# Kernel optimization log

Hardware: AMD Instinct MI355X
Metric: run time of the kernel (lower is better)

## Reference

```python
import jax, jax.numpy as jnp
import numpy as np

N = 16384   # nodes
E = 262144  # edges (avg degree 16)
H = 256     # hidden_dim
R = 32      # num_radial


def _lin(k, fi, fo):
    return jax.random.normal(k, (fi, fo), jnp.float32) / np.float32(np.sqrt(fi))


def setup_inputs() -> dict:
    key = jax.random.key(0)
    ks = jax.random.split(key, 16)
    h = jax.random.normal(ks[0], (N, H), jnp.float32)
    pos = jax.random.normal(ks[1], (N, 3), jnp.float32)
    edge_index = jax.random.randint(ks[2], (2, E), 0, N, dtype=jnp.int32)
    return {
        'h': h, 'pos': pos,
        # radial_basis: Linear(1,R), SiLU, Linear(R,R)
        'rb_w1': _lin(ks[3], 1, R), 'rb_b1': jnp.zeros((R,), jnp.float32),
        'rb_w2': _lin(ks[4], R, R), 'rb_b2': jnp.zeros((R,), jnp.float32),
        # edge_network: Linear(2H+R,H), SiLU, Linear(H,H), LayerNorm(H)
        'en_w1': _lin(ks[5], 2 * H + R, H), 'en_b1': jnp.zeros((H,), jnp.float32),
        'en_w2': _lin(ks[6], H, H), 'en_b2': jnp.zeros((H,), jnp.float32),
        'en_g': jnp.ones((H,), jnp.float32), 'en_bt': jnp.zeros((H,), jnp.float32),
        # node_network: Linear(2H,H), SiLU, Linear(H,H), LayerNorm(H)
        'nn_w1': _lin(ks[7], 2 * H, H), 'nn_b1': jnp.zeros((H,), jnp.float32),
        'nn_w2': _lin(ks[8], H, H), 'nn_b2': jnp.zeros((H,), jnp.float32),
        'nn_g': jnp.ones((H,), jnp.float32), 'nn_bt': jnp.zeros((H,), jnp.float32),
        # coord_network: Linear(H,H//2), SiLU, Linear(H//2,1), Tanh
        'cn_w1': _lin(ks[9], H, H // 2), 'cn_b1': jnp.zeros((H // 2,), jnp.float32),
        'cn_w2': _lin(ks[10], H // 2, 1), 'cn_b2': jnp.zeros((1,), jnp.float32),
        'edge_index': edge_index,
    }


def _ln(x, g, b, eps=1e-5):
    mu = jnp.mean(x, axis=-1, keepdims=True)
    var = jnp.var(x, axis=-1, keepdims=True)
    return (x - mu) / jnp.sqrt(var + eps) * g + b


def reference(h, pos, rb_w1, rb_b1, rb_w2, rb_b2,
              en_w1, en_b1, en_w2, en_b2, en_g, en_bt,
              nn_w1, nn_b1, nn_w2, nn_b2, nn_g, nn_bt,
              cn_w1, cn_b1, cn_w2, cn_b2, edge_index):
    row, col = edge_index[0], edge_index[1]
    rel_pos = pos[col] - pos[row]                                   # [E,3]
    # torch: norm(rel_pos + 1e-8) -> scalar eps added to the vector first
    dist = jnp.linalg.norm(rel_pos + 1e-8, axis=-1, keepdims=True)  # [E,1]
    radial = jax.nn.silu(dist @ rb_w1 + rb_b1) @ rb_w2 + rb_b2      # [E,R]
    edge_feat = jnp.concatenate([h[row], h[col], radial], axis=-1)  # [E,2H+R]
    edge_msg = _ln(jax.nn.silu(edge_feat @ en_w1 + en_b1) @ en_w2 + en_b2,
                   en_g, en_bt)                                     # [E,H]
    # PyG propagate with aggr='add': sum messages at target nodes (col)
    node_msg = jax.ops.segment_sum(edge_msg, col, num_segments=h.shape[0])
    hn_in = jnp.concatenate([h, node_msg], axis=-1)                 # [N,2H]
    h_updated = _ln(jax.nn.silu(hn_in @ nn_w1 + nn_b1) @ nn_w2 + nn_b2,
                    nn_g, nn_bt)                                    # [N,H]
    coord_w = jnp.tanh(jax.nn.silu(edge_msg @ cn_w1 + cn_b1) @ cn_w2 + cn_b2)  # [E,1]
    weighted = rel_pos * coord_w                                    # [E,3]
    pos_updates = jnp.zeros_like(pos).at[row].add(-weighted).at[col].add(weighted)
    return h_updated, pos_updates
```

## Files before the change

kernel.cpp:

```cpp
#include <hip/hip_runtime.h>
#include <hip/hip_bf16.h>


#define NN 16384
#define EE 262144
#define HH 256
#define RR 32

typedef __bf16 bf16x8 __attribute__((ext_vector_type(8)));
typedef float f32x4 __attribute__((ext_vector_type(4)));

__device__ __forceinline__ float silu_f(float x) { return x / (1.0f + __expf(-x)); }

__device__ __forceinline__ unsigned short bf_bits(float x) {
  union { __hip_bfloat16 b; unsigned short u; } v;
  v.b = __float2bfloat16(x);
  return v.u;
}
__device__ __forceinline__ float ubf(unsigned short u) {
  return __uint_as_float(((unsigned)u) << 16);
}

__global__ __launch_bounds__(256) void prep_all_kernel(
    const float* __restrict__ h, const int* __restrict__ ei,
    const float* __restrict__ en_w1, const float* __restrict__ en_w2,
    const float* __restrict__ nn_w1, const float* __restrict__ nn_w2,
    const float* __restrict__ cn_w1, const float* __restrict__ rb_w2,
    const float* __restrict__ rb_b2, const float* __restrict__ en_b1,
    __hip_bfloat16* __restrict__ hb, __hip_bfloat16* __restrict__ W2T,
    __hip_bfloat16* __restrict__ NW1T, __hip_bfloat16* __restrict__ NW2T,
    __hip_bfloat16* __restrict__ CW1T, __hip_bfloat16* __restrict__ W1abT,
    __hip_bfloat16* __restrict__ RWT, float* __restrict__ b1p,
    int* __restrict__ counts) {
  int bid = blockIdx.x, tid = threadIdx.x;
  if (bid < 4096) {
    int i = bid * 256 + tid;
    float4 v = ((const float4*)h)[i];
    __hip_bfloat16* d = hb + (size_t)i * 4;
    d[0] = __float2bfloat16(v.x);
    d[1] = __float2bfloat16(v.y);
    d[2] = __float2bfloat16(v.z);
    d[3] = __float2bfloat16(v.w);
    return;
  }
  if (bid < 5120) {
    int e = (bid - 4096) * 256 + tid;
    atomicAdd(&counts[ei[EE + e]], 1);
    return;
  }
  int b2 = bid - 5120;
  if (b2 < 256) {
    int i = b2 * 256 + tid, k = i >> 8, c = i & 255;
    W2T[(size_t)c * 256 + k] = __float2bfloat16(en_w2[i]);
  } else if (b2 < 768) {
    int i = (b2 - 256) * 256 + tid, k = i >> 8, c = i & 255;
    NW1T[(size_t)c * 512 + k] = __float2bfloat16(nn_w1[i]);
  } else if (b2 < 1024) {
    int i = (b2 - 768) * 256 + tid, k = i >> 8, c = i & 255;
    NW2T[(size_t)c * 256 + k] = __float2bfloat16(nn_w2[i]);
  } else if (b2 < 1152) {
    int i = (b2 - 1024) * 256 + tid, k = i >> 7, c = i & 127;
    CW1T[(size_t)c * 256 + k] = __float2bfloat16(cn_w1[i]);
  } else if (b2 < 1408) {
    int i = (b2 - 1152) * 256 + tid, k = i >> 8, c = i & 255;
    W1abT[(size_t)c * 256 + k] = __float2bfloat16(en_w1[i]);
  } else if (b2 < 1664) {
    int i = (b2 - 1408) * 256 + tid, k = i >> 8, c = i & 255;
    W1abT[(size_t)(256 + c) * 256 + k] = __float2bfloat16(en_w1[256 * 256 + i]);
  } else if (b2 < 1696) {
    int t = (b2 - 1664) * 256 + tid;
    int c = t >> 5, i = t & 31;
    float s = 0.f;
#pragma unroll
    for (int j = 0; j < 32; ++j) s += rb_w2[i * 32 + j] * en_w1[(512 + j) * 256 + c];
    RWT[c * 32 + i] = __float2bfloat16(s);
  } else {
    int c = tid;
    float s = en_b1[c];
#pragma unroll
    for (int j = 0; j < 32; ++j) s += rb_b2[j] * en_w1[(512 + j) * 256 + c];
    b1p[c] = s;
  }
}

__global__ __launch_bounds__(256) void scanA_kernel(const int* __restrict__ counts,
                                                    int* __restrict__ bsum) {
  __shared__ int ws[4];
  int t = threadIdx.x;
  int v = counts[blockIdx.x * 256 + t];
#pragma unroll
  for (int m = 1; m < 64; m <<= 1) v += __shfl_xor(v, m, 64);
  if ((t & 63) == 0) ws[t >> 6] = v;
  __syncthreads();
  if (t == 0) bsum[blockIdx.x] = ws[0] + ws[1] + ws[2] + ws[3];
}

__global__ __launch_bounds__(64) void scanB_kernel(const int* __restrict__ bsum,
                                                   int* __restrict__ bbase,
                                                   int* __restrict__ offs) {
  int t = threadIdx.x;
  int v = bsum[t], x = v;
#pragma unroll
  for (int d = 1; d < 64; d <<= 1) {
    int y = __shfl_up(x, d, 64);
    if (t >= d) x += y;
  }
  bbase[t] = x - v;
  if (t == 63) offs[NN] = x;
}

__global__ __launch_bounds__(256) void scanC_kernel(const int* __restrict__ counts,
                                                    const int* __restrict__ bbase,
                                                    int* __restrict__ offs,
                                                    int* __restrict__ cursor) {
  __shared__ int wtot[4];
  int t = threadIdx.x, wv = t >> 6, ln = t & 63;
  int base = blockIdx.x * 256;
  int v = counts[base + t], x = v;
#pragma unroll
  for (int d = 1; d < 64; d <<= 1) {
    int y = __shfl_up(x, d, 64);
    if (ln >= d) x += y;
  }
  if (ln == 63) wtot[wv] = x;
  __syncthreads();
  int add = bbase[blockIdx.x];
  for (int k = 0; k < wv; ++k) add += wtot[k];
  int excl = add + x - v;
  offs[base + t] = excl;
  cursor[base + t] = excl;
}

__global__ __launch_bounds__(256) void scatter_kernel(const int* __restrict__ ei,
                                                      int* __restrict__ cursor,
                                                      int* __restrict__ elist) {
  int e = blockIdx.x * 256 + threadIdx.x;
  if (e >= EE) return;
  int c = ei[EE + e];
  int p = atomicAdd(&cursor[c], 1);
  elist[p] = e;
}

__global__ __launch_bounds__(512) void pgemm_kernel(const __hip_bfloat16* __restrict__ A,
                                                    const __hip_bfloat16* __restrict__ BT,
                                                    __hip_bfloat16* __restrict__ out) {
  const int tid = threadIdx.x, w = tid >> 6, l = tid & 63, r = l & 15, g = l >> 4;
  const int n0 = blockIdx.x * 64;
  f32x4 acc[4][4];
#pragma unroll
  for (int a = 0; a < 4; ++a)
#pragma unroll
    for (int b = 0; b < 4; ++b) acc[a][b] = (f32x4){0.f, 0.f, 0.f, 0.f};
  for (int ks = 0; ks < 8; ++ks) {
    bf16x8 af[4], bfr[4];
#pragma unroll
    for (int fm = 0; fm < 4; ++fm)
      af[fm] = *(const bf16x8*)(A + (size_t)(n0 + fm * 16 + r) * 256 + ks * 32 + g * 8);
#pragma unroll
    for (int fn = 0; fn < 4; ++fn)
      bfr[fn] = *(const bf16x8*)(BT + (size_t)(w * 64 + fn * 16 + r) * 256 + ks * 32 + g * 8);
#pragma unroll
    for (int fm = 0; fm < 4; ++fm)
#pragma unroll
      for (int fn = 0; fn < 4; ++fn)
        acc[fm][fn] =
            __builtin_amdgcn_mfma_f32_16x16x32_bf16(af[fm], bfr[fn], acc[fm][fn], 0, 0, 0);
  }
#pragma unroll
  for (int fm = 0; fm < 4; ++fm)
#pragma unroll
    for (int fn = 0; fn < 4; ++fn) {
      int col = w * 64 + fn * 16 + r;
#pragma unroll
      for (int q = 0; q < 4; ++q) {
        int row = n0 + fm * 16 + g * 4 + q;
        out[(size_t)row * 512 + col] = __float2bfloat16(acc[fm][fn][q]);
      }
    }
}

__global__ __launch_bounds__(512, 4) void edge_kernel(
    const __hip_bfloat16* __restrict__ Pb, const int* __restrict__ ei,
    const float* __restrict__ pos, const float* __restrict__ rb_w1,
    const float* __restrict__ rb_b1, const __hip_bfloat16* __restrict__ RWT,
    const float* __restrict__ b1p, const __hip_bfloat16* __restrict__ W2T,
    const float* __restrict__ en_b2, const float* __restrict__ en_g,
    const float* __restrict__ en_bt, const __hip_bfloat16* __restrict__ CW1T,
    const float* __restrict__ cn_b1, const float* __restrict__ cn_w2,
    const float* __restrict__ cn_b2, const int* __restrict__ elist,
    float* __restrict__ nmsg, float* __restrict__ pos_out) {
  __shared__ __align__(16) __hip_bfloat16 A2[128 * 264];
  __shared__ float distb[128];
  __shared__ int srow[128], scol[128];
  __shared__ float red[8][128], redsq[8][128];
  __shared__ float mv[128][2];
  __shared__ float cb1b[128], cw2b[128];

  const int tid = threadIdx.x, w = tid >> 6, l = tid & 63, r = l & 15, g = l >> 4;
  const int e0 = blockIdx.x * 128;

  if (tid < 128) {
    cb1b[tid] = cn_b1[tid];
    cw2b[tid] = cn_w2[tid];
  }
  if (tid < 128) {
    int e = elist[e0 + tid];
    int r2 = ei[e], c2 = ei[EE + e];
    srow[tid] = r2;
    scol[tid] = c2;
    float ex = pos[c2 * 3 + 0] - pos[r2 * 3 + 0] + 1e-8f;
    float ey = pos[c2 * 3 + 1] - pos[r2 * 3 + 1] + 1e-8f;
    float ez = pos[c2 * 3 + 2] - pos[r2 * 3 + 2] + 1e-8f;
    distb[tid] = sqrtf(ex * ex + ey * ey + ez * ez);
  }
  __syncthreads();

  unsigned short* A2u = (unsigned short*)A2;
  {
    const int eloc = w * 16 + r;
    float d = distb[eloc];
    bf16x8 sfrag;
#pragma unroll
    for (int j = 0; j < 8; ++j) {
      float x = d * rb_w1[g * 8 + j] + rb_b1[g * 8 + j];
      sfrag[j] = (__bf16)silu_f(x);
    }
#pragma unroll
    for (int t = 0; t < 16; ++t) {
      int cbase = t * 16 + g * 4;
      bf16x8 afr = *(const bf16x8*)(RWT + (size_t)(t * 16 + r) * 32 + g * 8);
      f32x4 rad = __builtin_amdgcn_mfma_f32_16x16x32_bf16(
          afr, sfrag, (f32x4){0.f, 0.f, 0.f, 0.f}, 0, 0, 0);
      ushort4 o;
      o.x = bf_bits(rad[0]);
      o.y = bf_bits(rad[1]);
      o.z = bf_bits(rad[2]);
      o.w = bf_bits(rad[3]);
      *(ushort4*)(A2u + (size_t)eloc * 264 + cbase) = o;
    }
  }
  __syncthreads();

#pragma unroll
  for (int it = 0; it < 8; ++it) {
    int ch = it * 512 + tid;
    int i = ch >> 5, c = ch & 31;
    bf16x8 radv = *(const bf16x8*)(A2 + i * 264 + c * 8);
    bf16x8 p1 = *(const bf16x8*)(Pb + (size_t)srow[i] * 512 + c * 8);
    bf16x8 p2 = *(const bf16x8*)(Pb + (size_t)scol[i] * 512 + 256 + c * 8);
    float4 b1a = *(const float4*)(b1p + c * 8);
    float4 b1b = *(const float4*)(b1p + c * 8 + 4);
    float bv[8] = {b1a.x, b1a.y, b1a.z, b1a.w, b1b.x, b1b.y, b1b.z, b1b.w};
    bf16x8 o;
#pragma unroll
    for (int j = 0; j < 8; ++j)
      o[j] = (__bf16)silu_f((float)radv[j] + (float)p1[j] + (float)p2[j] + bv[j]);
    *(bf16x8*)(A2 + i * 264 + c * 8) = o;
  }
  __syncthreads();

  f32x4 acc[2][8];
#pragma unroll
  for (int a = 0; a < 2; ++a)
#pragma unroll
    for (int b = 0; b < 8; ++b) acc[a][b] = (f32x4){0.f, 0.f, 0.f, 0.f};
  for (int ks = 0; ks < 8; ++ks) {
    bf16x8 af[2], bfr[8];
#pragma unroll
    for (int mf = 0; mf < 2; ++mf)
      af[mf] = *(const bf16x8*)(W2T + (size_t)(w * 32 + mf * 16 + r) * 256 + ks * 32 + g * 8);
#pragma unroll
    for (int nf = 0; nf < 8; ++nf)
      bfr[nf] = *(const bf16x8*)(A2 + (nf * 16 + r) * 264 + ks * 32 + g * 8);
#pragma unroll
    for (int mf = 0; mf < 2; ++mf)
#pragma unroll
      for (int nf = 0; nf < 8; ++nf)
        acc[mf][nf] =
            __builtin_amdgcn_mfma_f32_16x16x32_bf16(af[mf], bfr[nf], acc[mf][nf], 0, 0, 0);
  }
  {
    float4 b2v0 = *(const float4*)(en_b2 + w * 32 + g * 4);
    float4 b2v1 = *(const float4*)(en_b2 + w * 32 + 16 + g * 4);
#pragma unroll
    for (int nf = 0; nf < 8; ++nf) {
      acc[0][nf][0] += b2v0.x;
      acc[0][nf][1] += b2v0.y;
      acc[0][nf][2] += b2v0.z;
      acc[0][nf][3] += b2v0.w;
      acc[1][nf][0] += b2v1.x;
      acc[1][nf][1] += b2v1.y;
      acc[1][nf][2] += b2v1.z;
      acc[1][nf][3] += b2v1.w;
    }
  }

#pragma unroll
  for (int nf = 0; nf < 8; ++nf) {
    float s = 0.f, sq = 0.f;
#pragma unroll
    for (int mf = 0; mf < 2; ++mf)
#pragma unroll
      for (int q = 0; q < 4; ++q) {
        float v = acc[mf][nf][q];
        s += v;
        sq += v * v;
      }
    s += __shfl_xor(s, 16, 64);
    s += __shfl_xor(s, 32, 64);
    sq += __shfl_xor(sq, 16, 64);
    sq += __shfl_xor(sq, 32, 64);
    if (l < 16) {
      red[w][nf * 16 + l] = s;
      redsq[w][nf * 16 + l] = sq;
    }
  }
  __syncthreads();
  if (tid < 128) {
    float s = 0.f, sq = 0.f;
#pragma unroll
    for (int k = 0; k < 8; ++k) {
      s += red[k][tid];
      sq += redsq[k][tid];
    }
    float mean = s * (1.0f / HH);
    float var = sq * (1.0f / HH) - mean * mean;
    mv[tid][0] = mean;
    mv[tid][1] = rsqrtf(var + 1e-5f);
  }
  __syncthreads();

  {
    float4 gv0 = *(const float4*)(en_g + w * 32 + g * 4);
    float4 gv1 = *(const float4*)(en_g + w * 32 + 16 + g * 4);
    float4 bv0 = *(const float4*)(en_bt + w * 32 + g * 4);
    float4 bv1 = *(const float4*)(en_bt + w * 32 + 16 + g * 4);
#pragma unroll
    for (int nf = 0; nf < 8; ++nf) {
      int e = nf * 16 + r;
      float mm = mv[e][0], rs = mv[e][1];
      ushort4 o0, o1;
      o0.x = bf_bits((acc[0][nf][0] - mm) * rs * gv0.x + bv0.x);
      o0.y = bf_bits((acc[0][nf][1] - mm) * rs * gv0.y + bv0.y);
      o0.z = bf_bits((acc[0][nf][2] - mm) * rs * gv0.z + bv0.z);
      o0.w = bf_bits((acc[0][nf][3] - mm) * rs * gv0.w + bv0.w);
      o1.x = bf_bits((acc[1][nf][0] - mm) * rs * gv1.x + bv1.x);
      o1.y = bf_bits((acc[1][nf][1] - mm) * rs * gv1.y + bv1.y);
      o1.z = bf_bits((acc[1][nf][2] - mm) * rs * gv1.z + bv1.z);
      o1.w = bf_bits((acc[1][nf][3] - mm) * rs * gv1.w + bv1.w);
      *(ushort4*)(A2u + (size_t)e * 264 + w * 32 + g * 4) = o0;
      *(ushort4*)(A2u + (size_t)e * 264 + w * 32 + 16 + g * 4) = o1;
    }
  }
  __syncthreads();

  {
    int c = tid & 255, h = tid >> 8;
    int rbeg = h * 64, rend = rbeg + 64;
    int segstart = rbeg;
    int cur = scol[rbeg];
    float run = 0.f;
    for (int row = rbeg; row < rend; ++row) {
      int nd = scol[row];
      if (nd != cur) {
        float* dst = &nmsg[(size_t)cur * 256 + c];
        if (segstart > rbeg)
          *dst = run;
        else
          atomicAdd(dst, run);
        segstart = row;
        cur = nd;
        run = 0.f;
      }
      run += ubf(A2u[(size_t)row * 264 + c]);
    }
    atomicAdd(&nmsg[(size_t)cur * 256 + c], run);
  }

  f32x4 c2a[8];
#pragma unroll
  for (int a = 0; a < 8; ++a) c2a[a] = (f32x4){0.f, 0.f, 0.f, 0.f};
  for (int ks = 0; ks < 8; ++ks) {
    bf16x8 bfr = *(const bf16x8*)(CW1T + (size_t)(w * 16 + r) * 256 + ks * 32 + g * 8);
#pragma unroll
    for (int fm = 0; fm < 8; ++fm) {
      bf16x8 af = *(const bf16x8*)(A2 + (fm * 16 + r) * 264 + ks * 32 + g * 8);
      c2a[fm] = __builtin_amdgcn_mfma_f32_16x16x32_bf16(af, bfr, c2a[fm], 0, 0, 0);
    }
  }
  {
    int ccol = w * 16 + r;
    float cb = cb1b[ccol], cw = cw2b[ccol];
#pragma unroll
    for (int fm = 0; fm < 8; ++fm)
#pragma unroll
      for (int q = 0; q < 4; ++q) {
        float v = silu_f(c2a[fm][q] + cb) * cw;
#pragma unroll
        for (int m = 1; m < 16; m <<= 1) v += __shfl_xor(v, m, 64);
        if (r == 0) red[w][fm * 16 + g * 4 + q] = v;
      }
  }
  __syncthreads();
  if (tid < 128) {
    float s = cn_b2[0];
#pragma unroll
    for (int k = 0; k < 8; ++k) s += red[k][tid];
    float wgt = tanhf(s);
    int rr = srow[tid], cc = scol[tid];
    float ax = pos[cc * 3 + 0] - pos[rr * 3 + 0];
    float ay = pos[cc * 3 + 1] - pos[rr * 3 + 1];
    float az = pos[cc * 3 + 2] - pos[rr * 3 + 2];
    atomicAdd(&pos_out[rr * 3 + 0], -wgt * ax);
    atomicAdd(&pos_out[rr * 3 + 1], -wgt * ay);
    atomicAdd(&pos_out[rr * 3 + 2], -wgt * az);
    atomicAdd(&pos_out[cc * 3 + 0], wgt * ax);
    atomicAdd(&pos_out[cc * 3 + 1], wgt * ay);
    atomicAdd(&pos_out[cc * 3 + 2], wgt * az);
  }
}

__global__ __launch_bounds__(512, 4) void node_kernel(
    const __hip_bfloat16* __restrict__ hb, const float* __restrict__ nmsg,
    const __hip_bfloat16* __restrict__ NW1T, const float* __restrict__ nn_b1,
    const __hip_bfloat16* __restrict__ NW2T, const float* __restrict__ nn_b2,
    const float* __restrict__ nn_g, const float* __restrict__ nn_bt,
    float* __restrict__ out_h) {
  __shared__ __align__(16) __hip_bfloat16 A2[64 * 264];
  __shared__ float red[8][64], redsq[8][64];
  __shared__ float mv[64][2];
  __shared__ float gb[HH], btb[HH];
  const int tid = threadIdx.x, w = tid >> 6, l = tid & 63, r = l & 15, g = l >> 4;
  const int n0 = blockIdx.x * 64;
  if (tid < 256) {
    gb[tid] = nn_g[tid];
    btb[tid] = nn_bt[tid];
  }

  f32x4 acc[4][2];
#pragma unroll
  for (int a = 0; a < 4; ++a)
#pragma unroll
    for (int b = 0; b < 2; ++b) acc[a][b] = (f32x4){0.f, 0.f, 0.f, 0.f};
  for (int ks = 0; ks < 8; ++ks) {
    bf16x8 af[4], bfr[2];
#pragma unroll
    for (int fm = 0; fm < 4; ++fm)
      af[fm] = *(const bf16x8*)(hb + (size_t)(n0 + fm * 16 + r) * 256 + ks * 32 + g * 8);
#pragma unroll
    for (int fn = 0; fn < 2; ++fn)
      bfr[fn] = *(const bf16x8*)(NW1T + (size_t)(w * 32 + fn * 16 + r) * 512 + ks * 32 + g * 8);
#pragma unroll
    for (int fm = 0; fm < 4; ++fm)
#pragma unroll
      for (int fn = 0; fn < 2; ++fn)
        acc[fm][fn] =
            __builtin_amdgcn_mfma_f32_16x16x32_bf16(af[fm], bfr[fn], acc[fm][fn], 0, 0, 0);
  }
  for (int ks = 0; ks < 8; ++ks) {
    bf16x8 af[4], bfr[2];
#pragma unroll
    for (int fm = 0; fm < 4; ++fm) {
      const float* src = nmsg + (size_t)(n0 + fm * 16 + r) * 256 + ks * 32 + g * 8;
      float4 a0 = *(const float4*)src;
      float4 a1 = *(const float4*)(src + 4);
      bf16x8 v;
      v[0] = (__bf16)a0.x;
      v[1] = (__bf16)a0.y;
      v[2] = (__bf16)a0.z;
      v[3] = (__bf16)a0.w;
      v[4] = (__bf16)a1.x;
      v[5] = (__bf16)a1.y;
      v[6] = (__bf16)a1.z;
      v[7] = (__bf16)a1.w;
      af[fm] = v;
    }
#pragma unroll
    for (int fn = 0; fn < 2; ++fn)
      bfr[fn] =
          *(const bf16x8*)(NW1T + (size_t)(w * 32 + fn * 16 + r) * 512 + 256 + ks * 32 + g * 8);
#pragma unroll
    for (int fm = 0; fm < 4; ++fm)
#pragma unroll
      for (int fn = 0; fn < 2; ++fn)
        acc[fm][fn] =
            __builtin_amdgcn_mfma_f32_16x16x32_bf16(af[fm], bfr[fn], acc[fm][fn], 0, 0, 0);
  }
  __syncthreads();
#pragma unroll
  for (int fn = 0; fn < 2; ++fn) {
    int col = w * 32 + fn * 16 + r;
    float b1 = nn_b1[col];
#pragma unroll
    for (int fm = 0; fm < 4; ++fm)
#pragma unroll
      for (int q = 0; q < 4; ++q) {
        int row = fm * 16 + g * 4 + q;
        A2[row * 264 + col] = __float2bfloat16(silu_f(acc[fm][fn][q] + b1));
      }
  }
  __syncthreads();

#pragma unroll
  for (int a = 0; a < 4; ++a)
#pragma unroll
    for (int b = 0; b < 2; ++b) acc[a][b] = (f32x4){0.f, 0.f, 0.f, 0.f};
  for (int ks = 0; ks < 8; ++ks) {
    bf16x8 af[4], bfr[2];
#pragma unroll
    for (int fm = 0; fm < 4; ++fm)
      af[fm] = *(const bf16x8*)(A2 + (fm * 16 + r) * 264 + ks * 32 + g * 8);
#pragma unroll
    for (int fn = 0; fn < 2; ++fn)
      bfr[fn] = *(const bf16x8*)(NW2T + (size_t)(w * 32 + fn * 16 + r) * 256 + ks * 32 + g * 8);
#pragma unroll
    for (int fm = 0; fm < 4; ++fm)
#pragma unroll
      for (int fn = 0; fn < 2; ++fn)
        acc[fm][fn] =
            __builtin_amdgcn_mfma_f32_16x16x32_bf16(af[fm], bfr[fn], acc[fm][fn], 0, 0, 0);
  }
#pragma unroll
  for (int fn = 0; fn < 2; ++fn) {
    float b2 = nn_b2[w * 32 + fn * 16 + r];
#pragma unroll
    for (int fm = 0; fm < 4; ++fm)
#pragma unroll
      for (int q = 0; q < 4; ++q) acc[fm][fn][q] += b2;
  }
#pragma unroll
  for (int fm = 0; fm < 4; ++fm)
#pragma unroll
    for (int q = 0; q < 4; ++q) {
      float s = acc[fm][0][q] + acc[fm][1][q];
      float sq = acc[fm][0][q] * acc[fm][0][q] + acc[fm][1][q] * acc[fm][1][q];
#pragma unroll
      for (int m = 1; m < 16; m <<= 1) {
        s += __shfl_xor(s, m, 64);
        sq += __shfl_xor(sq, m, 64);
      }
      if (r == 0) {
        red[w][fm * 16 + g * 4 + q] = s;
        redsq[w][fm * 16 + g * 4 + q] = sq;
      }
    }
  __syncthreads();
  if (tid < 64) {
    float s = 0.f, sq = 0.f;
#pragma unroll
    for (int k = 0; k < 8; ++k) {
      s += red[k][tid];
      sq += redsq[k][tid];
    }
    float mean = s * (1.0f / HH);
    float var = sq * (1.0f / HH) - mean * mean;
    mv[tid][0] = mean;
    mv[tid][1] = rsqrtf(var + 1e-5f);
  }
  __syncthreads();
#pragma unroll
  for (int fn = 0; fn < 2; ++fn) {
    int col = w * 32 + fn * 16 + r;
    float gg = gb[col], bb = btb[col];
#pragma unroll
    for (int fm = 0; fm < 4; ++fm)
#pragma unroll
      for (int q = 0; q < 4; ++q) {
        int row = fm * 16 + g * 4 + q;
        out_h[(size_t)(n0 + row) * HH + col] =
            (acc[fm][fn][q] - mv[row][0]) * mv[row][1] * gg + bb;
      }
  }
}

extern "C" void kernel_launch(void* const* d_in, const int* in_sizes, int n_in,
                              void* d_out, int out_size, void* d_ws, size_t ws_size,
                              hipStream_t stream) {
  const float* h = (const float*)d_in[0];
  const float* pos = (const float*)d_in[1];
  const float* rb_w1 = (const float*)d_in[2];
  const float* rb_b1 = (const float*)d_in[3];
  const float* rb_w2 = (const float*)d_in[4];
  const float* rb_b2 = (const float*)d_in[5];
  const float* en_w1 = (const float*)d_in[6];
  const float* en_b1 = (const float*)d_in[7];
  const float* en_w2 = (const float*)d_in[8];
  const float* en_b2 = (const float*)d_in[9];
  const float* en_g = (const float*)d_in[10];
  const float* en_bt = (const float*)d_in[11];
  const float* nn_w1 = (const float*)d_in[12];
  const float* nn_b1 = (const float*)d_in[13];
  const float* nn_w2 = (const float*)d_in[14];
  const float* nn_b2 = (const float*)d_in[15];
  const float* nn_g = (const float*)d_in[16];
  const float* nn_bt = (const float*)d_in[17];
  const float* cn_w1 = (const float*)d_in[18];
  const float* cn_b1 = (const float*)d_in[19];
  const float* cn_w2 = (const float*)d_in[20];
  const float* cn_b2 = (const float*)d_in[21];
  const int* ei = (const int*)d_in[22];

  float* out_h = (float*)d_out;
  float* out_pos = out_h + (size_t)NN * HH;

  char* p = (char*)d_ws;
  auto alloc = [&p](size_t bytes) {
    char* q = p;
    p += (bytes + 255) & ~(size_t)255;
    return q;
  };
  __hip_bfloat16* hb = (__hip_bfloat16*)alloc((size_t)NN * HH * 2);
  __hip_bfloat16* Pb = (__hip_bfloat16*)alloc((size_t)NN * 512 * 2);
  __hip_bfloat16* W1abT = (__hip_bfloat16*)alloc((size_t)512 * 256 * 2);
  __hip_bfloat16* W2T = (__hip_bfloat16*)alloc((size_t)256 * 256 * 2);
  __hip_bfloat16* NW1T = (__hip_bfloat16*)alloc((size_t)256 * 512 * 2);
  __hip_bfloat16* NW2T = (__hip_bfloat16*)alloc((size_t)256 * 256 * 2);
  __hip_bfloat16* CW1T = (__hip_bfloat16*)alloc((size_t)128 * 256 * 2);
  __hip_bfloat16* RWT = (__hip_bfloat16*)alloc((size_t)256 * 32 * 2);
  float* b1p = (float*)alloc((size_t)256 * 4);
  float* nmsg = (float*)alloc((size_t)NN * HH * 4);
  int* counts = (int*)alloc((size_t)NN * 4);
  int* offs = (int*)alloc((size_t)(NN + 1) * 4);
  int* cursor = (int*)alloc((size_t)NN * 4);
  int* elist = (int*)alloc((size_t)EE * 4);
  int* bsum = (int*)alloc((size_t)64 * 4);
  int* bbase = (int*)alloc((size_t)64 * 4);

  hipMemsetAsync(out_pos, 0, (size_t)NN * 3 * sizeof(float), stream);
  hipMemsetAsync(counts, 0, (size_t)NN * sizeof(int), stream);
  hipMemsetAsync(nmsg, 0, (size_t)NN * HH * sizeof(float), stream);

  prep_all_kernel<<<6817, 256, 0, stream>>>(h, ei, en_w1, en_w2, nn_w1, nn_w2, cn_w1, rb_w2,
                                            rb_b2, en_b1, hb, W2T, NW1T, NW2T, CW1T, W1abT,
                                            RWT, b1p, counts);
  scanA_kernel<<<NN / 256, 256, 0, stream>>>(counts, bsum);
  scanB_kernel<<<1, 64, 0, stream>>>(bsum, bbase, offs);
  scanC_kernel<<<NN / 256, 256, 0, stream>>>(counts, bbase, offs, cursor);
  scatter_kernel<<<EE / 256, 256, 0, stream>>>(ei, cursor, elist);
  pgemm_kernel<<<NN / 64, 512, 0, stream>>>(hb, W1abT, Pb);
  edge_kernel<<<EE / 128, 512, 0, stream>>>(Pb, ei, pos, rb_w1, rb_b1, RWT, b1p, W2T, en_b2,
                                            en_g, en_bt, CW1T, cn_b1, cn_w2, cn_b2, elist,
                                            nmsg, out_pos);
  node_kernel<<<NN / 64, 512, 0, stream>>>(hb, nmsg, NW1T, nn_b1, NW2T, nn_b2, nn_g, nn_bt,
                                           out_h);
}
```

Before: 444.9 us.

## Drop bf16 copy of h, merge scan stages and fuse scatter into pgemm

Removes the separate pass that converted h to bf16; the projection GEMM and node kernel now load fp32 h and convert to bf16 in registers. The single-block scanB is folded into scanC, with every block redoing the 64-element prefix scan. The edge scatter is merged with the projection GEMM into one launch using a split on block index. This cuts two kernel launches and one full write plus reread of h, at the cost of twice the global read bytes for h inside the GEMMs.

```diff
diff --git a/kernel.cpp b/kernel.cpp
--- a/kernel.cpp
+++ b/kernel.cpp
@@ -21,34 +21,38 @@
   return __uint_as_float(((unsigned)u) << 16);
 }
 
+__device__ __forceinline__ bf16x8 cvt8(const float* src) {
+  float4 a0 = *(const float4*)src;
+  float4 a1 = *(const float4*)(src + 4);
+  bf16x8 v;
+  v[0] = (__bf16)a0.x;
+  v[1] = (__bf16)a0.y;
+  v[2] = (__bf16)a0.z;
+  v[3] = (__bf16)a0.w;
+  v[4] = (__bf16)a1.x;
+  v[5] = (__bf16)a1.y;
+  v[6] = (__bf16)a1.z;
+  v[7] = (__bf16)a1.w;
+  return v;
+}
+
 __global__ __launch_bounds__(256) void prep_all_kernel(
-    const float* __restrict__ h, const int* __restrict__ ei,
-    const float* __restrict__ en_w1, const float* __restrict__ en_w2,
-    const float* __restrict__ nn_w1, const float* __restrict__ nn_w2,
-    const float* __restrict__ cn_w1, const float* __restrict__ rb_w2,
-    const float* __restrict__ rb_b2, const float* __restrict__ en_b1,
-    __hip_bfloat16* __restrict__ hb, __hip_bfloat16* __restrict__ W2T,
+    const int* __restrict__ ei, const float* __restrict__ en_w1,
+    const float* __restrict__ en_w2, const float* __restrict__ nn_w1,
+    const float* __restrict__ nn_w2, const float* __restrict__ cn_w1,
+    const float* __restrict__ rb_w2, const float* __restrict__ rb_b2,
+    const float* __restrict__ en_b1, __hip_bfloat16* __restrict__ W2T,
     __hip_bfloat16* __restrict__ NW1T, __hip_bfloat16* __restrict__ NW2T,
     __hip_bfloat16* __restrict__ CW1T, __hip_bfloat16* __restrict__ W1abT,
     __hip_bfloat16* __restrict__ RWT, float* __restrict__ b1p,
     int* __restrict__ counts) {
   int bid = blockIdx.x, tid = threadIdx.x;
-  if (bid < 4096) {
-    int i = bid * 256 + tid;
-    float4 v = ((const float4*)h)[i];
-    __hip_bfloat16* d = hb + (size_t)i * 4;
-    d[0] = __float2bfloat16(v.x);
-    d[1] = __float2bfloat16(v.y);
-    d[2] = __float2bfloat16(v.z);
-    d[3] = __float2bfloat16(v.w);
-    return;
-  }
-  if (bid < 5120) {
-    int e = (bid - 4096) * 256 + tid;
+  if (bid < 1024) {
+    int e = bid * 256 + tid;
     atomicAdd(&counts[ei[EE + e]], 1);
     return;
   }
-  int b2 = bid - 5120;
+  int b2 = bid - 1024;
   if (b2 < 256) {
     int i = b2 * 256 + tid, k = i >> 8, c = i & 255;
     W2T[(size_t)c * 256 + k] = __float2bfloat16(en_w2[i]);
@@ -95,26 +99,23 @@
   if (t == 0) bsum[blockIdx.x] = ws[0] + ws[1] + ws[2] + ws[3];
 }
 
-__global__ __launch_bounds__(64) void scanB_kernel(const int* __restrict__ bsum,
-                                                   int* __restrict__ bbase,
-                                                   int* __restrict__ offs) {
-  int t = threadIdx.x;
-  int v = bsum[t], x = v;
-#pragma unroll
-  for (int d = 1; d < 64; d <<= 1) {
-    int y = __shfl_up(x, d, 64);
-    if (t >= d) x += y;
-  }
-  bbase[t] = x - v;
-  if (t == 63) offs[NN] = x;
-}
-
-__global__ __launch_bounds__(256) void scanC_kernel(const int* __restrict__ counts,
-                                                    const int* __restrict__ bbase,
-                                                    int* __restrict__ offs,
-                                                    int* __restrict__ cursor) {
+__global__ __launch_bounds__(256) void scanBC_kernel(const int* __restrict__ counts,
+                                                     const int* __restrict__ bsum,
+                                                     int* __restrict__ offs,
+                                                     int* __restrict__ cursor) {
   __shared__ int wtot[4];
+  __shared__ int baseSh;
   int t = threadIdx.x, wv = t >> 6, ln = t & 63;
+  if (t < 64) {
+    int v = bsum[t], x = v;
+#pragma unroll
+    for (int d = 1; d < 64; d <<= 1) {
+      int y = __shfl_up(x, d, 64);
+      if (t >= d) x += y;
+    }
+    if (t == (int)blockIdx.x) baseSh = x - v;
+    if (blockIdx.x == 0 && t == 63) offs[NN] = x;
+  }
   int base = blockIdx.x * 256;
   int v = counts[base + t], x = v;
 #pragma unroll
@@ -124,28 +125,26 @@
   }
   if (ln == 63) wtot[wv] = x;
   __syncthreads();
-  int add = bbase[blockIdx.x];
+  int add = baseSh;
   for (int k = 0; k < wv; ++k) add += wtot[k];
   int excl = add + x - v;
   offs[base + t] = excl;
   cursor[base + t] = excl;
 }
 
-__global__ __launch_bounds__(256) void scatter_kernel(const int* __restrict__ ei,
-                                                      int* __restrict__ cursor,
-                                                      int* __restrict__ elist) {
-  int e = blockIdx.x * 256 + threadIdx.x;
-  if (e >= EE) return;
-  int c = ei[EE + e];
-  int p = atomicAdd(&cursor[c], 1);
-  elist[p] = e;
-}
-
-__global__ __launch_bounds__(512) void pgemm_kernel(const __hip_bfloat16* __restrict__ A,
-                                                    const __hip_bfloat16* __restrict__ BT,
-                                                    __hip_bfloat16* __restrict__ out) {
+__global__ __launch_bounds__(512) void scatter_pgemm_kernel(
+    const int* __restrict__ ei, int* __restrict__ cursor, int* __restrict__ elist,
+    const float* __restrict__ h, const __hip_bfloat16* __restrict__ BT,
+    __hip_bfloat16* __restrict__ out) {
+  if (blockIdx.x < 512) {
+    int e = blockIdx.x * 512 + threadIdx.x;
+    int c = ei[EE + e];
+    int p = atomicAdd(&cursor[c], 1);
+    elist[p] = e;
+    return;
+  }
   const int tid = threadIdx.x, w = tid >> 6, l = tid & 63, r = l & 15, g = l >> 4;
-  const int n0 = blockIdx.x * 64;
+  const int n0 = (blockIdx.x - 512) * 64;
   f32x4 acc[4][4];
 #pragma unroll
   for (int a = 0; a < 4; ++a)
@@ -155,7 +154,7 @@
     bf16x8 af[4], bfr[4];
 #pragma unroll
     for (int fm = 0; fm < 4; ++fm)
-      af[fm] = *(const bf16x8*)(A + (size_t)(n0 + fm * 16 + r) * 256 + ks * 32 + g * 8);
+      af[fm] = cvt8(h + (size_t)(n0 + fm * 16 + r) * 256 + ks * 32 + g * 8);
 #pragma unroll
     for (int fn = 0; fn < 4; ++fn)
       bfr[fn] = *(const bf16x8*)(BT + (size_t)(w * 64 + fn * 16 + r) * 256 + ks * 32 + g * 8);
@@ -355,8 +354,8 @@
   __syncthreads();
 
   {
-    int c = tid & 255, h = tid >> 8;
-    int rbeg = h * 64, rend = rbeg + 64;
+    int c = tid & 255, h2 = tid >> 8;
+    int rbeg = h2 * 64, rend = rbeg + 64;
     int segstart = rbeg;
     int cur = scol[rbeg];
     float run = 0.f;
@@ -421,7 +420,7 @@
 }
 
 __global__ __launch_bounds__(512, 4) void node_kernel(
-    const __hip_bfloat16* __restrict__ hb, const float* __restrict__ nmsg,
+    const float* __restrict__ h, const float* __restrict__ nmsg,
     const __hip_bfloat16* __restrict__ NW1T, const float* __restrict__ nn_b1,
     const __hip_bfloat16* __restrict__ NW2T, const float* __restrict__ nn_b2,
     const float* __restrict__ nn_g, const float* __restrict__ nn_bt,
@@ -446,7 +445,7 @@
     bf16x8 af[4], bfr[2];
 #pragma unroll
     for (int fm = 0; fm < 4; ++fm)
-      af[fm] = *(const bf16x8*)(hb + (size_t)(n0 + fm * 16 + r) * 256 + ks * 32 + g * 8);
+      af[fm] = cvt8(h + (size_t)(n0 + fm * 16 + r) * 256 + ks * 32 + g * 8);
 #pragma unroll
     for (int fn = 0; fn < 2; ++fn)
       bfr[fn] = *(const bf16x8*)(NW1T + (size_t)(w * 32 + fn * 16 + r) * 512 + ks * 32 + g * 8);
@@ -460,21 +459,8 @@
   for (int ks = 0; ks < 8; ++ks) {
     bf16x8 af[4], bfr[2];
 #pragma unroll
-    for (int fm = 0; fm < 4; ++fm) {
-      const float* src = nmsg + (size_t)(n0 + fm * 16 + r) * 256 + ks * 32 + g * 8;
-      float4 a0 = *(const float4*)src;
-      float4 a1 = *(const float4*)(src + 4);
-      bf16x8 v;
-      v[0] = (__bf16)a0.x;
-      v[1] = (__bf16)a0.y;
-      v[2] = (__bf16)a0.z;
-      v[3] = (__bf16)a0.w;
-      v[4] = (__bf16)a1.x;
-      v[5] = (__bf16)a1.y;
-      v[6] = (__bf16)a1.z;
-      v[7] = (__bf16)a1.w;
-      af[fm] = v;
-    }
+    for (int fm = 0; fm < 4; ++fm)
+      af[fm] = cvt8(nmsg + (size_t)(n0 + fm * 16 + r) * 256 + ks * 32 + g * 8);
 #pragma unroll
     for (int fn = 0; fn < 2; ++fn)
       bfr[fn] =
@@ -609,7 +595,6 @@
     p += (bytes + 255) & ~(size_t)255;
     return q;
   };
-  __hip_bfloat16* hb = (__hip_bfloat16*)alloc((size_t)NN * HH * 2);
   __hip_bfloat16* Pb = (__hip_bfloat16*)alloc((size_t)NN * 512 * 2);
   __hip_bfloat16* W1abT = (__hip_bfloat16*)alloc((size_t)512 * 256 * 2);
   __hip_bfloat16* W2T = (__hip_bfloat16*)alloc((size_t)256 * 256 * 2);
@@ -624,23 +609,20 @@
   int* cursor = (int*)alloc((size_t)NN * 4);
   int* elist = (int*)alloc((size_t)EE * 4);
   int* bsum = (int*)alloc((size_t)64 * 4);
-  int* bbase = (int*)alloc((size_t)64 * 4);
 
   hipMemsetAsync(out_pos, 0, (size_t)NN * 3 * sizeof(float), stream);
   hipMemsetAsync(counts, 0, (size_t)NN * sizeof(int), stream);
   hipMemsetAsync(nmsg, 0, (size_t)NN * HH * sizeof(float), stream);
 
-  prep_all_kernel<<<6817, 256, 0, stream>>>(h, ei, en_w1, en_w2, nn_w1, nn_w2, cn_w1, rb_w2,
-                                            rb_b2, en_b1, hb, W2T, NW1T, NW2T, CW1T, W1abT,
-                                            RWT, b1p, counts);
+  prep_all_kernel<<<2721, 256, 0, stream>>>(ei, en_w1, en_w2, nn_w1, nn_w2, cn_w1, rb_w2,
+                                            rb_b2, en_b1, W2T, NW1T, NW2T, CW1T, W1abT, RWT,
+                                            b1p, counts);
   scanA_kernel<<<NN / 256, 256, 0, stream>>>(counts, bsum);
-  scanB_kernel<<<1, 64, 0, stream>>>(bsum, bbase, offs);
-  scanC_kernel<<<NN / 256, 256, 0, stream>>>(counts, bbase, offs, cursor);
-  scatter_kernel<<<EE / 256, 256, 0, stream>>>(ei, cursor, elist);
-  pgemm_kernel<<<NN / 64, 512, 0, stream>>>(hb, W1abT, Pb);
+  scanBC_kernel<<<NN / 256, 256, 0, stream>>>(counts, bsum, offs, cursor);
+  scatter_pgemm_kernel<<<512 + NN / 64, 512, 0, stream>>>(ei, cursor, elist, h, W1abT, Pb);
   edge_kernel<<<EE / 128, 512, 0, stream>>>(Pb, ei, pos, rb_w1, rb_b1, RWT, b1p, W2T, en_b2,
                                             en_g, en_bt, CW1T, cn_b1, cn_w2, cn_b2, elist,
                                             nmsg, out_pos);
-  node_kernel<<<NN / 64, 512, 0, stream>>>(hb, nmsg, NW1T, nn_b1, NW2T, nn_b2, nn_g, nn_bt,
+  node_kernel<<<NN / 64, 512, 0, stream>>>(h, nmsg, NW1T, nn_b1, NW2T, nn_b2, nn_g, nn_bt,
                                            out_h);
 }
```

Result: slower. 474.6 us (+6.7%).
